# Performance work log

Hardware: AMD Instinct MI355X
Metric: run time of the kernel (lower is better)

## Reference

```python
import jax, jax.numpy as jnp
from jax import lax
import numpy as np

STYLE_STRENGTH = 1.0
PATCH = 3
TOL = 1e-14


def covsqrt_mean(feature, inverse=False):
    # feature: [b, c, h, w]; matches torch covsqrt_mean with eigenvalue truncation.
    b, c, h, w = feature.shape
    f = feature.reshape(b, c, h * w)
    mean = jnp.mean(f, axis=2, keepdims=True)
    zm = f - mean
    cov = jnp.einsum('bcn,bdn->bcd', zm, zm)  # unnormalized covariance, [b,c,c]
    evals, evecs = jnp.linalg.eigh(cov)       # ascending evals, like torch
    p = -0.5 if inverse else 0.5
    # torch keeps evals[k:] where k is the first index with eval > tol; since
    # evals are sorted ascending this equals masking evals > tol.
    mask = evals > TOL
    d = jnp.where(mask, jnp.where(mask, evals, 1.0) ** p, 0.0)
    covsqrt = jnp.einsum('bij,bj,bkj->bik', evecs, d, evecs)
    return covsqrt, mean


def whitening(feature):
    b, c, h, w = feature.shape
    inv_cs, mean = covsqrt_mean(feature, inverse=True)
    out = jnp.einsum('bcd,bdn->bcn', inv_cs, feature.reshape(b, c, -1) - mean)
    return out.reshape(b, c, h, w)


def coloring(feature, target):
    b, c, h, w = feature.shape
    cs, mean = covsqrt_mean(target, inverse=False)
    out = jnp.einsum('bcd,bdn->bcn', cs, feature.reshape(b, c, -1)) + mean
    return out.reshape(b, c, h, w)


def extract_kernels(feat, k):
    # feat [b,c,h,w] -> per-location style patches as conv kernels [b, h*w, c, k, k]
    b, c, h, w = feat.shape
    pad = (k - 1) // 2
    fp = jnp.pad(feat, ((0, 0), (0, 0), (pad, pad), (pad, pad)))
    # stack the k*k shifted views: [b, c, h, w, k*k] in (ky, kx) row-major order,
    # matching torch unfold(2,k).unfold(3,k) flattening.
    patches = jnp.stack([fp[:, :, dy:dy + h, dx:dx + w]
                         for dy in range(k) for dx in range(k)], axis=-1)
    return patches.reshape(b, c, h * w, k * k).transpose(0, 2, 1, 3).reshape(b, h * w, c, k, k)


def reassemble(norm_c, norm_s, k):
    b, c, h, w = norm_c.shape
    ker = extract_kernels(norm_s, k)                                  # [b, hw_s, c, k, k]
    knorm = jnp.sqrt(jnp.sum(ker ** 2, axis=(2, 3, 4), keepdims=True))
    pad = (k - 1) // 2

    def conv_one(feat, kk):
        # feat [c,h,w], kk [hw_s,c,k,k] -> score [hw_s,h,w]
        x = jnp.pad(feat, ((0, 0), (pad, pad), (pad, pad)))[None]
        return lax.conv_general_dilated(x, kk, (1, 1), 'VALID')[0]

    score = jax.vmap(conv_one)(norm_c, ker / knorm)                   # [b, hw_s, h, w]
    idx = jnp.argmax(score, axis=1)                                   # [b, h, w]
    onehot = jax.nn.one_hot(idx, score.shape[1], dtype=score.dtype).transpose(0, 3, 1, 2)

    def deconv_one(oh, kk):
        # conv_transpose2d(padded onehot, kk, padding=k-1) == VALID conv with
        # spatially flipped kernel (in/out channels swapped).
        x = jnp.pad(oh, ((0, 0), (pad, pad), (pad, pad)))[None]        # [1, hw_s, h+2p, w+2p]
        wf = jnp.flip(kk, axis=(2, 3)).transpose(1, 0, 2, 3)           # [c, hw_s, k, k]
        return lax.conv_general_dilated(x, wf, (1, 1), 'VALID')[0]     # [c, h, w]

    out = jax.vmap(deconv_one)(onehot, ker)                           # [b, c, h, w]
    # overlap-count normalization: separable box filter of ones
    cnt_h = jnp.convolve(jnp.ones(h, out.dtype), jnp.ones(k, out.dtype), mode='same')
    cnt_w = jnp.convolve(jnp.ones(w, out.dtype), jnp.ones(k, out.dtype), mode='same')
    deconv_norm = (cnt_h[:, None] * cnt_w[None, :])[None, None]
    return out / deconv_norm


def setup_inputs() -> dict:
    key = jax.random.key(0)
    k1, k2 = jax.random.split(key)
    b, ch, h, w = 2, 256, 48, 48
    c = jax.random.normal(k1, (b, ch, h, w), dtype=jnp.float32)
    s = jax.random.normal(k2, (b, ch, h, w), dtype=jnp.float32)
    return {'c': c, 's': s}


def reference(c, s):
    norm_c = whitening(c)
    norm_s = whitening(s)
    rF = reassemble(norm_c, norm_s, PATCH)
    sF = coloring(rF, s)
    return (1.0 - STYLE_STRENGTH) * c + STYLE_STRENGTH * sF
```

## Files before the change

kernel.cpp:

```cpp
#include <hip/hip_runtime.h>
#include <math.h>

#define HW 2304
#define NC 256
#define NPIX 2500
#define NPIXP 2560
#define MATSZ 65536
#define NS_ITERS 5
#define NSLAB 6
#define KSLAB 384
#define PMSZ (2560 * 256)
#define GSZ ((u64)NPIXP * NPIXP)

typedef unsigned long long u64;
typedef unsigned short ushortt;
typedef __attribute__((ext_vector_type(8))) short bhalf8;
typedef __attribute__((ext_vector_type(4))) float f32x4;

__global__ void mean_kernel(const float* __restrict__ c, const float* __restrict__ s,
                            double* __restrict__ mean, double* __restrict__ snorm) {
  int ch = blockIdx.x, m = blockIdx.y;
  const float* src = (m < 2 ? c + m * (NC * HW) : s + (m - 2) * (NC * HW)) + ch * HW;
  double acc = 0.0, acc2 = 0.0;
  for (int n = threadIdx.x; n < HW; n += 64) {
    double v = (double)src[n];
    acc += v; acc2 += v * v;
  }
  for (int o = 32; o > 0; o >>= 1) {
    acc += __shfl_down(acc, o);
    acc2 += __shfl_down(acc2, o);
  }
  if (threadIdx.x == 0) {
    mean[m * NC + ch] = acc / (double)HW;
    double diag = acc2 - acc * acc / (double)HW;
    atomicAdd(&snorm[m], 1.25 * diag / 256.0);
  }
}

__launch_bounds__(256)
__global__ void cov_part(const float* __restrict__ c, const float* __restrict__ s,
                         float* __restrict__ covp) {
  int z = blockIdx.z;
  int m = z / NSLAB, slab = z % NSLAB;
  const float* src = (m < 2 ? c + m * (NC * HW) : s + (m - 2) * (NC * HW));
  int i0 = blockIdx.y * 64, j0 = blockIdx.x * 64;
  int kb = slab * KSLAB;
  __shared__ float As[16][64], Bs[16][64];
  int tx = threadIdx.x, ty = threadIdx.y;
  int tid = ty * 16 + tx;
  int li = tid >> 2;
  int lk4 = tid & 3;
  float acc[4][4] = {};
  for (int kc = 0; kc < KSLAB; kc += 16) {
    __syncthreads();
    float4 va = *(const float4*)&src[(u64)(i0 + li) * HW + kb + kc + lk4 * 4];
    float4 vb = *(const float4*)&src[(u64)(j0 + li) * HW + kb + kc + lk4 * 4];
    As[lk4 * 4 + 0][li] = va.x; As[lk4 * 4 + 1][li] = va.y;
    As[lk4 * 4 + 2][li] = va.z; As[lk4 * 4 + 3][li] = va.w;
    Bs[lk4 * 4 + 0][li] = vb.x; Bs[lk4 * 4 + 1][li] = vb.y;
    Bs[lk4 * 4 + 2][li] = vb.z; Bs[lk4 * 4 + 3][li] = vb.w;
    __syncthreads();
    #pragma unroll
    for (int kk = 0; kk < 16; ++kk) {
      float4 a = *(const float4*)&As[kk][ty * 4];
      float4 b = *(const float4*)&Bs[kk][tx * 4];
      float av[4] = {a.x, a.y, a.z, a.w};
      float bv[4] = {b.x, b.y, b.z, b.w};
      #pragma unroll
      for (int i = 0; i < 4; ++i)
        #pragma unroll
        for (int j = 0; j < 4; ++j) acc[i][j] += av[i] * bv[j];
    }
  }
  float* Cp = covp + (u64)z * MATSZ;
  #pragma unroll
  for (int i = 0; i < 4; ++i) {
    float4 v = make_float4(acc[i][0], acc[i][1], acc[i][2], acc[i][3]);
    *(float4*)&Cp[(i0 + ty * 4 + i) * NC + j0 + tx * 4] = v;
  }
}

__global__ void cov_reduce(const float* __restrict__ covp, const double* __restrict__ mean,
                           const double* __restrict__ snorm,
                           float* __restrict__ Y0, float* __restrict__ Z1) {
  int m = blockIdx.y;
  int row = blockIdx.x, col = threadIdx.x;
  int e = row * 256 + col;
  float v = 0.0f;
  #pragma unroll
  for (int slab = 0; slab < NSLAB; ++slab)
    v += covp[(u64)(m * NSLAB + slab) * MATSZ + e];
  double mi = mean[m * NC + row], mj = mean[m * NC + col];
  float res = (float)((double)v - (double)HW * mi * mj);
  float inv = (float)(1.0 / snorm[m]);
  float y0 = res * inv;
  Y0[m * MATSZ + e] = y0;
  Z1[m * MATSZ + e] = ((row == col) ? 1.5f : 0.0f) - 0.5f * y0;
}

__launch_bounds__(256)
__global__ void ns_gemm_Y(const float* __restrict__ Y0, const float* __restrict__ T0,
                          float* __restrict__ Y1) {
  int m = blockIdx.z;
  const float* A = Y0 + m * MATSZ;
  const float* B = T0 + m * MATSZ;
  float* Cp = Y1 + m * MATSZ;
  int m0 = blockIdx.y * 32, n0 = blockIdx.x * 32;
  __shared__ float As[32][33], Bs[32][33];
  int tx = threadIdx.x, ty = threadIdx.y;
  int tid = ty * 16 + tx;
  float acc[2][2] = {};
  for (int k0 = 0; k0 < 256; k0 += 32) {
    __syncthreads();
    #pragma unroll
    for (int l = 0; l < 4; ++l) {
      int idx = tid + l * 256;
      int r = idx >> 5, cc = idx & 31;
      As[r][cc] = A[(m0 + r) * NC + k0 + cc];
      Bs[r][cc] = B[(k0 + r) * NC + n0 + cc];
    }
    __syncthreads();
    #pragma unroll
    for (int kk = 0; kk < 32; ++kk) {
      float a0 = As[ty][kk], a1 = As[ty + 16][kk];
      float b0 = Bs[kk][tx], b1 = Bs[kk][tx + 16];
      acc[0][0] += a0 * b0; acc[0][1] += a0 * b1;
      acc[1][0] += a1 * b0; acc[1][1] += a1 * b1;
    }
  }
  #pragma unroll
  for (int i = 0; i < 2; ++i)
    #pragma unroll
    for (int j = 0; j < 2; ++j)
      Cp[(m0 + ty + 16 * i) * NC + n0 + tx + 16 * j] = acc[i][j];
}

__launch_bounds__(256)
__global__ void ns_gemm_T(const float* __restrict__ Zc, const float* __restrict__ Yc,
                          float* __restrict__ T) {
  int m = blockIdx.z;
  const float* A = Zc + m * MATSZ;
  const float* B = Yc + m * MATSZ;
  int m0 = blockIdx.y * 32, n0 = blockIdx.x * 32;
  __shared__ float As[32][33], Bs[32][33];
  int tx = threadIdx.x, ty = threadIdx.y;
  int tid = ty * 16 + tx;
  float acc[2][2] = {};
  for (int k0 = 0; k0 < 256; k0 += 32) {
    __syncthreads();
    #pragma unroll
    for (int l = 0; l < 4; ++l) {
      int idx = tid + l * 256;
      int r = idx >> 5, cc = idx & 31;
      As[r][cc] = A[(m0 + r) * NC + k0 + cc];
      Bs[r][cc] = B[(k0 + r) * NC + n0 + cc];
    }
    __syncthreads();
    #pragma unroll
    for (int kk = 0; kk < 32; ++kk) {
      float a0 = As[ty][kk], a1 = As[ty + 16][kk];
      float b0 = Bs[kk][tx], b1 = Bs[kk][tx + 16];
      acc[0][0] += a0 * b0; acc[0][1] += a0 * b1;
      acc[1][0] += a1 * b0; acc[1][1] += a1 * b1;
    }
  }
  float* Cp = T + m * MATSZ;
  #pragma unroll
  for (int i = 0; i < 2; ++i)
    #pragma unroll
    for (int j = 0; j < 2; ++j) {
      int row = m0 + ty + 16 * i, col = n0 + tx + 16 * j;
      Cp[row * NC + col] = (row == col ? 1.5f : 0.0f) - 0.5f * acc[i][j];
    }
}

__launch_bounds__(256)
__global__ void ns_gemm_YZ(const float* __restrict__ Yc, const float* __restrict__ Zc,
                           const float* __restrict__ T,
                           float* __restrict__ Yn, float* __restrict__ Zn) {
  int z = blockIdx.z;
  int m = z & 3;
  bool isY = (z < 4);
  const float* A = isY ? (Yc + m * MATSZ) : (T + m * MATSZ);
  const float* B = isY ? (T + m * MATSZ) : (Zc + m * MATSZ);
  float* Cp = isY ? (Yn + m * MATSZ) : (Zn + m * MATSZ);
  int m0 = blockIdx.y * 32, n0 = blockIdx.x * 32;
  __shared__ float As[32][33], Bs[32][33];
  int tx = threadIdx.x, ty = threadIdx.y;
  int tid = ty * 16 + tx;
  float acc[2][2] = {};
  for (int k0 = 0; k0 < 256; k0 += 32) {
    __syncthreads();
    #pragma unroll
    for (int l = 0; l < 4; ++l) {
      int idx = tid + l * 256;
      int r = idx >> 5, cc = idx & 31;
      As[r][cc] = A[(m0 + r) * NC + k0 + cc];
      Bs[r][cc] = B[(k0 + r) * NC + n0 + cc];
    }
    __syncthreads();
    #pragma unroll
    for (int kk = 0; kk < 32; ++kk) {
      float a0 = As[ty][kk], a1 = As[ty + 16][kk];
      float b0 = Bs[kk][tx], b1 = Bs[kk][tx + 16];
      acc[0][0] += a0 * b0; acc[0][1] += a0 * b1;
      acc[1][0] += a1 * b0; acc[1][1] += a1 * b1;
    }
  }
  #pragma unroll
  for (int i = 0; i < 2; ++i)
    #pragma unroll
    for (int j = 0; j < 2; ++j)
      Cp[(m0 + ty + 16 * i) * NC + n0 + tx + 16 * j] = acc[i][j];
}

__launch_bounds__(256)
__global__ void whiten_kernel(const float* __restrict__ c, const float* __restrict__ s,
                              const float* __restrict__ Zf,
                              const double* __restrict__ snorm, const double* __restrict__ mean,
                              float* __restrict__ padC_cf, float* __restrict__ padS_cf,
                              float* __restrict__ padS_cl) {
  int mat = blockIdx.z;
  const float* src = (mat < 2 ? c + mat * (NC * HW) : s + (mat - 2) * (NC * HW));
  const float* A = Zf + mat * MATSZ;
  const double* mn = mean + mat * NC;
  float wscale = (float)(1.0 / sqrt(snorm[mat]));
  int m0 = blockIdx.y * 64, n0 = blockIdx.x * 64;
  __shared__ float As[16][68], Bs[16][68];
  int tid = threadIdx.x;
  int tx = tid & 15, ty = tid >> 4;
  int li = tid >> 2, lk4 = tid & 3;
  int kr = tid >> 4, p4 = (tid & 15) * 4;
  float acc[4][4] = {};
  for (int kc = 0; kc < 256; kc += 16) {
    __syncthreads();
    float4 va = *(const float4*)&A[(u64)(m0 + li) * NC + kc + lk4 * 4];
    As[lk4 * 4 + 0][li] = va.x; As[lk4 * 4 + 1][li] = va.y;
    As[lk4 * 4 + 2][li] = va.z; As[lk4 * 4 + 3][li] = va.w;
    float mk = (float)mn[kc + kr];
    float4 vb = *(const float4*)&src[(u64)(kc + kr) * HW + n0 + p4];
    vb.x -= mk; vb.y -= mk; vb.z -= mk; vb.w -= mk;
    *(float4*)&Bs[kr][p4] = vb;
    __syncthreads();
    #pragma unroll
    for (int kk = 0; kk < 16; ++kk) {
      float4 a = *(const float4*)&As[kk][ty * 4];
      float4 b = *(const float4*)&Bs[kk][tx * 4];
      float av[4] = {a.x, a.y, a.z, a.w};
      float bv[4] = {b.x, b.y, b.z, b.w};
      #pragma unroll
      for (int i = 0; i < 4; ++i)
        #pragma unroll
        for (int j = 0; j < 4; ++j) acc[i][j] += av[i] * bv[j];
    }
  }
  #pragma unroll
  for (int i = 0; i < 4; ++i) {
    int row = m0 + ty * 4 + i;
    #pragma unroll
    for (int j = 0; j < 4; ++j) {
      int n = n0 + tx * 4 + j;
      float v = acc[i][j] * wscale;
      int y = n / 48, x = n % 48;
      int ppos = (y + 1) * 50 + (x + 1);
      if (mat < 2) {
        padC_cf[(u64)mat * (NC * NPIXP) + row * NPIXP + ppos] = v;
      } else {
        padS_cf[(u64)(mat - 2) * (NC * NPIXP) + row * NPIXP + ppos] = v;
        padS_cl[(u64)(mat - 2) * (NPIX * NC) + ppos * NC + row] = v;
      }
    }
  }
}

__launch_bounds__(256)
__global__ void tsplit_kernel(const float* __restrict__ padC_cf, const float* __restrict__ padS_cf,
                              ushortt* __restrict__ padCk_hi, ushortt* __restrict__ padCk_lo,
                              ushortt* __restrict__ padSk_hi, ushortt* __restrict__ padSk_lo,
                              float* __restrict__ ssq) {
  int p0 = blockIdx.x * 64;
  int by = blockIdx.y;
  const float* src = (by < 2) ? padC_cf + (u64)by * (NC * NPIXP)
                              : padS_cf + (u64)(by - 2) * (NC * NPIXP);
  ushortt* dhi = (by < 2) ? padCk_hi + (u64)by * PMSZ : padSk_hi + (u64)(by - 2) * PMSZ;
  ushortt* dlo = (by < 2) ? padCk_lo + (u64)by * PMSZ : padSk_lo + (u64)(by - 2) * PMSZ;
  __shared__ float Tk[64][68];
  int tid = threadIdx.x;
  int rr = tid >> 4, c4 = (tid & 15) * 4;
  int p = tid >> 2, kg = (tid & 3) * 16;
  float sq = 0.0f;
  for (int ks = 0; ks < 256; ks += 64) {
    __syncthreads();
    #pragma unroll
    for (int it = 0; it < 4; ++it) {
      int r = rr + it * 16;
      *(float4*)&Tk[r][c4] = *(const float4*)&src[(u64)(ks + r) * NPIXP + p0 + c4];
    }
    __syncthreads();
    __align__(16) ushortt h[16], lo[16];
    #pragma unroll
    for (int e = 0; e < 16; ++e) {
      float v = Tk[kg + e][p];
      sq += v * v;
      unsigned bb = __float_as_uint(v);
      unsigned hu = (bb + 0x7FFFu + ((bb >> 16) & 1u)) >> 16;
      float hf = __uint_as_float(hu << 16);
      float rres = v - hf;
      unsigned lb = __float_as_uint(rres);
      unsigned lu = (lb + 0x7FFFu + ((lb >> 16) & 1u)) >> 16;
      h[e] = (ushortt)hu;
      lo[e] = (ushortt)lu;
    }
    u64 off = (u64)(p0 + p) * 256 + ks + kg;
    *(uint4*)&dhi[off] = *(const uint4*)&h[0];
    *(uint4*)&dhi[off + 8] = *(const uint4*)&h[8];
    *(uint4*)&dlo[off] = *(const uint4*)&lo[0];
    *(uint4*)&dlo[off + 8] = *(const uint4*)&lo[8];
  }
  sq += __shfl_down(sq, 2);
  sq += __shfl_down(sq, 1);
  if (by >= 2 && (tid & 3) == 0 && (p0 + p) < NPIX)
    ssq[(u64)(by - 2) * NPIX + p0 + p] = sq;
}

__launch_bounds__(256)
__global__ void gram_mfma(const ushortt* __restrict__ Ah_b, const ushortt* __restrict__ Al_b,
                          const ushortt* __restrict__ Bh_b, const ushortt* __restrict__ Bl_b,
                          float* __restrict__ Gb) {
  int bz = blockIdx.z;
  const ushortt* Ah_g = Ah_b + (u64)bz * PMSZ;
  const ushortt* Al_g = Al_b + (u64)bz * PMSZ;
  const ushortt* Bh_g = Bh_b + (u64)bz * PMSZ;
  const ushortt* Bl_g = Bl_b + (u64)bz * PMSZ;
  float* G = Gb + (u64)bz * GSZ;
  __shared__ ushortt As_hi[128 * 32], As_lo[128 * 32], Bs_hi[64 * 32], Bs_lo[64 * 32];
  int tid = threadIdx.x;
  int wv = tid >> 6, l = tid & 63, lr = l & 15, lk = l >> 4;
  int p0 = blockIdx.x * 128, q0 = blockIdx.y * 64;
  int arow = tid >> 2;
  int apart = (tid & 3) * 8;
  const ushortt* pAh0 = Ah_g + (u64)(p0 + arow) * 256 + apart;
  const ushortt* pAh1 = Ah_g + (u64)(p0 + arow + 64) * 256 + apart;
  const ushortt* pAl0 = Al_g + (u64)(p0 + arow) * 256 + apart;
  const ushortt* pAl1 = Al_g + (u64)(p0 + arow + 64) * 256 + apart;
  const ushortt* pBh  = Bh_g + (u64)(q0 + arow) * 256 + apart;
  const ushortt* pBl  = Bl_g + (u64)(q0 + arow) * 256 + apart;
  float4 rAh0 = *(const float4*)pAh0;
  float4 rAh1 = *(const float4*)pAh1;
  float4 rAl0 = *(const float4*)pAl0;
  float4 rAl1 = *(const float4*)pAl1;
  float4 rBh  = *(const float4*)pBh;
  float4 rBl  = *(const float4*)pBl;
  f32x4 acc[2][4];
  #pragma unroll
  for (int a = 0; a < 2; ++a)
    #pragma unroll
    for (int b = 0; b < 4; ++b)
      #pragma unroll
      for (int e = 0; e < 4; ++e) acc[a][b][e] = 0.0f;
  for (int k0 = 0; k0 < 256; k0 += 32) {
    __syncthreads();
    *(float4*)&As_hi[arow * 32 + apart] = rAh0;
    *(float4*)&As_hi[(arow + 64) * 32 + apart] = rAh1;
    *(float4*)&As_lo[arow * 32 + apart] = rAl0;
    *(float4*)&As_lo[(arow + 64) * 32 + apart] = rAl1;
    *(float4*)&Bs_hi[arow * 32 + apart] = rBh;
    *(float4*)&Bs_lo[arow * 32 + apart] = rBl;
    __syncthreads();
    if (k0 + 32 < 256) {
      rAh0 = *(const float4*)(pAh0 + k0 + 32);
      rAh1 = *(const float4*)(pAh1 + k0 + 32);
      rAl0 = *(const float4*)(pAl0 + k0 + 32);
      rAl1 = *(const float4*)(pAl1 + k0 + 32);
      rBh  = *(const float4*)(pBh + k0 + 32);
      rBl  = *(const float4*)(pBl + k0 + 32);
    }
    bhalf8 Ah[2], Al[2], Bh[4], Bl[4];
    #pragma unroll
    for (int a = 0; a < 2; ++a) {
      int off = (wv * 32 + a * 16 + lr) * 32 + lk * 8;
      Ah[a] = *(const bhalf8*)&As_hi[off];
      Al[a] = *(const bhalf8*)&As_lo[off];
    }
    #pragma unroll
    for (int b = 0; b < 4; ++b) {
      int off = (b * 16 + lr) * 32 + lk * 8;
      Bh[b] = *(const bhalf8*)&Bs_hi[off];
      Bl[b] = *(const bhalf8*)&Bs_lo[off];
    }
    #pragma unroll
    for (int a = 0; a < 2; ++a)
      #pragma unroll
      for (int b = 0; b < 4; ++b) {
        acc[a][b] = __builtin_amdgcn_mfma_f32_16x16x32_bf16(Ah[a], Bh[b], acc[a][b], 0, 0, 0);
        acc[a][b] = __builtin_amdgcn_mfma_f32_16x16x32_bf16(Ah[a], Bl[b], acc[a][b], 0, 0, 0);
        acc[a][b] = __builtin_amdgcn_mfma_f32_16x16x32_bf16(Al[a], Bh[b], acc[a][b], 0, 0, 0);
      }
  }
  #pragma unroll
  for (int a = 0; a < 2; ++a)
    #pragma unroll
    for (int b = 0; b < 4; ++b)
      #pragma unroll
      for (int r = 0; r < 4; ++r) {
        int p = p0 + wv * 32 + a * 16 + lk * 4 + r;
        int q = q0 + b * 16 + lr;
        G[(u64)p * NPIXP + q] = acc[a][b][r];
      }
}

__launch_bounds__(256)
__global__ void scoremax_kernel(const float* __restrict__ Gb, const float* __restrict__ ssq,
                                u64* __restrict__ rmax) {
  int j = blockIdx.x, cidx = blockIdx.y, b = blockIdx.z;
  int c = cidx - 47;
  int y_lo = c < 0 ? -c : 0;
  int y_hi = c < 0 ? 47 : 47 - c;
  int yt0 = y_lo + j * 4;
  if (yt0 > y_hi) return;
  int ny = min(4, y_hi - yt0 + 1);
  int nb = ny + 2;
  const float* G = Gb + (u64)b * GSZ;
  const float* sq = ssq + (u64)b * NPIX;
  __shared__ float bands[6][2500];
  __shared__ float ssqb[6][52];
  __shared__ float sc[48][52];
  __shared__ float rkl[48];
  int tid = threadIdx.x;
  for (int e = tid; e < nb * 2500; e += 256) {
    int bi = e / 2500, rem = e - bi * 2500;
    int u = rem / 50, v = rem - u * 50;
    int a = yt0 + bi;
    bands[bi][rem] = G[(u64)(a * 50 + u) * NPIXP + (a + c) * 50 + v];
  }
  for (int e = tid; e < nb * 50; e += 256) {
    int bi = e / 50, v = e - bi * 50;
    ssqb[bi][v] = sq[(yt0 + bi + c) * 50 + v];
  }
  __syncthreads();
  for (int jj = 0; jj < ny; ++jj) {
    int y = yt0 + jj, ys = y + c;
    #pragma unroll
    for (int k = 0; k < 9; ++k) {
      int idx = tid + k * 256;
      int x = idx / 48, xs = idx - x * 48;
      float v = 0.0f;
      #pragma unroll
      for (int dy = 0; dy < 3; ++dy)
        #pragma unroll
        for (int dx = 0; dx < 3; ++dx)
          v += bands[jj + dy][(x + dx) * 50 + xs + dx];
      sc[x][xs] = v;
    }
    if (tid < 48) {
      float t = 0.0f;
      #pragma unroll
      for (int dy = 0; dy < 3; ++dy)
        #pragma unroll
        for (int dx = 0; dx < 3; ++dx) t += ssqb[jj + dy][tid + dx];
      rkl[tid] = 1.0f / sqrtf(t);
    }
    __syncthreads();
    if (tid < 192) {
      int r = tid >> 2, part = tid & 3;
      float best = -1e30f; int bxs = 0;
      #pragma unroll
      for (int i = 0; i < 12; ++i) {
        int xs = part * 12 + i;
        float v = sc[r][xs] * rkl[xs];
        if (v > best) { best = v; bxs = xs; }
      }
      #pragma unroll
      for (int o = 1; o < 4; o <<= 1) {
        float ov = __shfl_down(best, o);
        int oi = __shfl_down(bxs, o);
        if (ov > best || (ov == best && oi < bxs)) { best = ov; bxs = oi; }
      }
      if (part == 0) {
        int ps = ys * 48 + bxs;
        unsigned ub = __float_as_uint(best);
        unsigned enc = (ub & 0x80000000u) ? ~ub : (ub | 0x80000000u);
        u64 key = ((u64)enc << 32) | (u64)(2303 - ps);
        atomicMax(&rmax[(u64)b * HW + y * 48 + r], key);
      }
    }
    __syncthreads();
  }
}

__global__ void reassemble_kernel(const float* __restrict__ padS_cl, const u64* __restrict__ rmax,
                                  float* __restrict__ rF_cl) {
  int pix = blockIdx.x, b = blockIdx.y;
  int y = pix / 48, x = pix % 48;
  const u64* rm = rmax + (u64)b * HW;
  const float* S = padS_cl + (u64)b * (NPIX * NC);
  int ch = threadIdx.x;
  float sum = 0.0f;
  #pragma unroll
  for (int i = 0; i < 3; ++i)
    #pragma unroll
    for (int j = 0; j < 3; ++j) {
      int yn = y + 1 - i, xn = x + 1 - j;
      if (yn >= 0 && yn < 48 && xn >= 0 && xn < 48) {
        int ps = 2303 - (int)(unsigned)(rm[yn * 48 + xn] & 0xFFFFFFFFu);
        int ys = ps / 48, xs = ps % 48;
        sum += S[((ys + i) * 50 + xs + j) * NC + ch];
      }
    }
  float cy = (y == 0 || y == 47) ? 2.0f : 3.0f;
  float cx = (x == 0 || x == 47) ? 2.0f : 3.0f;
  rF_cl[(u64)b * (HW * NC) + pix * NC + ch] = sum / (cy * cx);
}

__launch_bounds__(256)
__global__ void coloring_kernel(const float* __restrict__ Yf, const double* __restrict__ snorm,
                                const double* __restrict__ mean, const float* __restrict__ rF_cl,
                                float* __restrict__ out) {
  int b = blockIdx.z;
  const float* A = Yf + (2 + b) * MATSZ;
  const float* Bp = rF_cl + (u64)b * (HW * NC);
  const double* mn = mean + (2 + b) * NC;
  float cscale = (float)sqrt(snorm[2 + b]);
  int m0 = blockIdx.y * 64, n0 = blockIdx.x * 64;
  __shared__ float As[16][68], Bs[16][68];
  int tid = threadIdx.x;
  int tx = tid & 15, ty = tid >> 4;
  int li = tid >> 2, lk4 = tid & 3;
  int pix = tid >> 2, kq = (tid & 3) * 4;
  float acc[4][4] = {};
  for (int kc = 0; kc < 256; kc += 16) {
    __syncthreads();
    float4 va = *(const float4*)&A[(u64)(m0 + li) * NC + kc + lk4 * 4];
    As[lk4 * 4 + 0][li] = va.x; As[lk4 * 4 + 1][li] = va.y;
    As[lk4 * 4 + 2][li] = va.z; As[lk4 * 4 + 3][li] = va.w;
    float4 vb = *(const float4*)&Bp[(u64)(n0 + pix) * NC + kc + kq];
    Bs[kq + 0][pix] = vb.x; Bs[kq + 1][pix] = vb.y;
    Bs[kq + 2][pix] = vb.z; Bs[kq + 3][pix] = vb.w;
    __syncthreads();
    #pragma unroll
    for (int kk = 0; kk < 16; ++kk) {
      float4 a = *(const float4*)&As[kk][ty * 4];
      float4 b2 = *(const float4*)&Bs[kk][tx * 4];
      float av[4] = {a.x, a.y, a.z, a.w};
      float bv[4] = {b2.x, b2.y, b2.z, b2.w};
      #pragma unroll
      for (int i = 0; i < 4; ++i)
        #pragma unroll
        for (int j = 0; j < 4; ++j) acc[i][j] += av[i] * bv[j];
    }
  }
  #pragma unroll
  for (int i = 0; i < 4; ++i) {
    int row = m0 + ty * 4 + i;
    float madd = (float)mn[row];
    float4 v = make_float4(acc[i][0] * cscale + madd, acc[i][1] * cscale + madd,
                           acc[i][2] * cscale + madd, acc[i][3] * cscale + madd);
    *(float4*)&out[(u64)b * (NC * HW) + (u64)row * HW + n0 + tx * 4] = v;
  }
}

extern "C" void kernel_launch(void* const* d_in, const int* in_sizes, int n_in,
                              void* d_out, int out_size, void* d_ws, size_t ws_size,
                              hipStream_t stream) {
  const float* c = (const float*)d_in[0];
  const float* s = (const float*)d_in[1];
  float* out = (float*)d_out;

  char* ws = (char*)d_ws;
  size_t off = 0;
  auto alloc = [&](size_t bytes) {
    void* p = ws + off;
    off = (off + bytes + 255) & ~(size_t)255;
    return p;
  };
  double* mean   = (double*)alloc(4 * NC * sizeof(double));
  float* covp    = (float*)alloc((size_t)4 * NSLAB * MATSZ * sizeof(float));
  float* Ya      = (float*)alloc((size_t)4 * MATSZ * sizeof(float));
  float* Yb      = (float*)alloc((size_t)4 * MATSZ * sizeof(float));
  float* Za      = (float*)alloc((size_t)4 * MATSZ * sizeof(float));
  float* Zb      = (float*)alloc((size_t)4 * MATSZ * sizeof(float));
  float* T       = (float*)alloc((size_t)4 * MATSZ * sizeof(float));
  float* padC_cf = (float*)alloc((size_t)2 * NC * NPIXP * sizeof(float));
  float* padS_cf = (float*)alloc((size_t)2 * NC * NPIXP * sizeof(float));
  float* padS_cl = (float*)alloc((size_t)2 * NPIX * NC * sizeof(float));
  ushortt* padCk_hi = (ushortt*)alloc((size_t)2 * PMSZ * sizeof(ushortt));
  ushortt* padCk_lo = (ushortt*)alloc((size_t)2 * PMSZ * sizeof(ushortt));
  ushortt* padSk_hi = (ushortt*)alloc((size_t)2 * PMSZ * sizeof(ushortt));
  ushortt* padSk_lo = (ushortt*)alloc((size_t)2 * PMSZ * sizeof(ushortt));
  float* ssq     = (float*)alloc((size_t)2 * NPIX * sizeof(float));
  float* rF_cl   = (float*)alloc((size_t)2 * HW * NC * sizeof(float));
  float* G       = (float*)alloc((size_t)2 * GSZ * sizeof(float));
  u64*   rmax    = (u64*)alloc((size_t)2 * HW * sizeof(u64));
  double* snorm  = (double*)alloc(4 * sizeof(double));

  size_t padBytes = (size_t)(2 * NC * NPIXP + 2 * NC * NPIXP + 2 * NPIX * NC) * sizeof(float);
  hipMemsetAsync(padC_cf, 0, padBytes, stream);
  hipMemsetAsync(rmax, 0, (size_t)2 * HW * sizeof(u64) + 4 * sizeof(double), stream);

  mean_kernel<<<dim3(256, 4), 64, 0, stream>>>(c, s, mean, snorm);
  cov_part<<<dim3(4, 4, 4 * NSLAB), dim3(16, 16), 0, stream>>>(c, s, covp);
  cov_reduce<<<dim3(256, 4), 256, 0, stream>>>(covp, mean, snorm, Ya, Za);
  ns_gemm_Y<<<dim3(8, 8, 4), dim3(16, 16), 0, stream>>>(Ya, Za, Yb);

  float *Yc = Yb, *Zc = Za, *Yn = Ya, *Zn = Zb;
  for (int it = 1; it < NS_ITERS; ++it) {
    ns_gemm_T<<<dim3(8, 8, 4), dim3(16, 16), 0, stream>>>(Zc, Yc, T);
    ns_gemm_YZ<<<dim3(8, 8, 8), dim3(16, 16), 0, stream>>>(Yc, Zc, T, Yn, Zn);
    float* t1 = Yc; Yc = Yn; Yn = t1;
    float* t2 = Zc; Zc = Zn; Zn = t2;
  }

  whiten_kernel<<<dim3(36, 4, 4), 256, 0, stream>>>(c, s, Zc, snorm, mean,
                                                    padC_cf, padS_cf, padS_cl);
  tsplit_kernel<<<dim3(40, 4), 256, 0, stream>>>(padC_cf, padS_cf,
                                                 padCk_hi, padCk_lo, padSk_hi, padSk_lo, ssq);

  gram_mfma<<<dim3(20, 40, 2), 256, 0, stream>>>(padCk_hi, padCk_lo, padSk_hi, padSk_lo, G);
  scoremax_kernel<<<dim3(12, 95, 2), 256, 0, stream>>>(G, ssq, rmax);

  reassemble_kernel<<<dim3(2304, 2), 256, 0, stream>>>(padS_cl, rmax, rF_cl);
  coloring_kernel<<<dim3(36, 4, 2), 256, 0, stream>>>(Yc, snorm, mean, rF_cl, out);
}
```

Before: 334.3 us.

## Restructure score-max kernel to one block per row pair with smaller LDS

The score-max kernel now assigns one block to each (content row, style row) pair instead of a diagonal band of up to four rows. It streams the three needed Gram tiles one at a time into a single shared buffer and accumulates the 3x3 patch score in place. This cuts shared memory per block sharply to raise occupancy and doubles the grid size. In exchange, each Gram tile is re-read from global memory more often, since the cross-row band reuse is lost.

```diff
diff --git a/kernel.cpp b/kernel.cpp
--- a/kernel.cpp
+++ b/kernel.cpp
@@ -412,79 +412,64 @@
 __launch_bounds__(256)
 __global__ void scoremax_kernel(const float* __restrict__ Gb, const float* __restrict__ ssq,
                                 u64* __restrict__ rmax) {
-  int j = blockIdx.x, cidx = blockIdx.y, b = blockIdx.z;
-  int c = cidx - 47;
-  int y_lo = c < 0 ? -c : 0;
-  int y_hi = c < 0 ? 47 : 47 - c;
-  int yt0 = y_lo + j * 4;
-  if (yt0 > y_hi) return;
-  int ny = min(4, y_hi - yt0 + 1);
-  int nb = ny + 2;
+  int y = blockIdx.x, ys = blockIdx.y, b = blockIdx.z;
   const float* G = Gb + (u64)b * GSZ;
   const float* sq = ssq + (u64)b * NPIX;
-  __shared__ float bands[6][2500];
-  __shared__ float ssqb[6][52];
+  __shared__ float Gt1[50][52];
   __shared__ float sc[48][52];
+  __shared__ float sr[152];
   __shared__ float rkl[48];
   int tid = threadIdx.x;
-  for (int e = tid; e < nb * 2500; e += 256) {
-    int bi = e / 2500, rem = e - bi * 2500;
-    int u = rem / 50, v = rem - u * 50;
-    int a = yt0 + bi;
-    bands[bi][rem] = G[(u64)(a * 50 + u) * NPIXP + (a + c) * 50 + v];
-  }
-  for (int e = tid; e < nb * 50; e += 256) {
-    int bi = e / 50, v = e - bi * 50;
-    ssqb[bi][v] = sq[(yt0 + bi + c) * 50 + v];
-  }
-  __syncthreads();
-  for (int jj = 0; jj < ny; ++jj) {
-    int y = yt0 + jj, ys = y + c;
+  for (int dy = 0; dy < 3; ++dy) {
+    if (dy > 0) __syncthreads();
+    for (int t = tid; t < 2500; t += 256) {
+      int u = t / 50, v = t - u * 50;
+      Gt1[u][v] = G[(u64)((y + dy) * 50 + u) * NPIXP + (ys + dy) * 50 + v];
+    }
+    if (dy == 0 && tid < 150) {
+      int d = tid / 50, v = tid - d * 50;
+      sr[d * 50 + v] = sq[(ys + d) * 50 + v];
+    }
+    __syncthreads();
+    if (dy == 0 && tid < 48) {
+      float t = 0.0f;
+      #pragma unroll
+      for (int d = 0; d < 3; ++d)
+        #pragma unroll
+        for (int dx = 0; dx < 3; ++dx) t += sr[d * 50 + tid + dx];
+      rkl[tid] = 1.0f / sqrtf(t);
+    }
     #pragma unroll
     for (int k = 0; k < 9; ++k) {
       int idx = tid + k * 256;
       int x = idx / 48, xs = idx - x * 48;
-      float v = 0.0f;
-      #pragma unroll
-      for (int dy = 0; dy < 3; ++dy)
-        #pragma unroll
-        for (int dx = 0; dx < 3; ++dx)
-          v += bands[jj + dy][(x + dx) * 50 + xs + dx];
-      sc[x][xs] = v;
-    }
-    if (tid < 48) {
-      float t = 0.0f;
-      #pragma unroll
-      for (int dy = 0; dy < 3; ++dy)
-        #pragma unroll
-        for (int dx = 0; dx < 3; ++dx) t += ssqb[jj + dy][tid + dx];
-      rkl[tid] = 1.0f / sqrtf(t);
-    }
-    __syncthreads();
-    if (tid < 192) {
-      int r = tid >> 2, part = tid & 3;
-      float best = -1e30f; int bxs = 0;
-      #pragma unroll
-      for (int i = 0; i < 12; ++i) {
-        int xs = part * 12 + i;
-        float v = sc[r][xs] * rkl[xs];
-        if (v > best) { best = v; bxs = xs; }
-      }
-      #pragma unroll
-      for (int o = 1; o < 4; o <<= 1) {
-        float ov = __shfl_down(best, o);
-        int oi = __shfl_down(bxs, o);
-        if (ov > best || (ov == best && oi < bxs)) { best = ov; bxs = oi; }
-      }
-      if (part == 0) {
-        int ps = ys * 48 + bxs;
-        unsigned ub = __float_as_uint(best);
-        unsigned enc = (ub & 0x80000000u) ? ~ub : (ub | 0x80000000u);
-        u64 key = ((u64)enc << 32) | (u64)(2303 - ps);
-        atomicMax(&rmax[(u64)b * HW + y * 48 + r], key);
-      }
-    }
-    __syncthreads();
+      float v = Gt1[x][xs] + Gt1[x + 1][xs + 1] + Gt1[x + 2][xs + 2];
+      sc[x][xs] = (dy == 0) ? v : sc[x][xs] + v;
+    }
+  }
+  __syncthreads();
+  if (tid < 192) {
+    int r = tid >> 2, part = tid & 3;
+    float best = -1e30f; int bxs = 0;
+    #pragma unroll
+    for (int i = 0; i < 12; ++i) {
+      int xs = part * 12 + i;
+      float v = sc[r][xs] * rkl[xs];
+      if (v > best) { best = v; bxs = xs; }
+    }
+    #pragma unroll
+    for (int o = 1; o < 4; o <<= 1) {
+      float ov = __shfl_down(best, o);
+      int oi = __shfl_down(bxs, o);
+      if (ov > best || (ov == best && oi < bxs)) { best = ov; bxs = oi; }
+    }
+    if (part == 0) {
+      int ps = ys * 48 + bxs;
+      unsigned ub = __float_as_uint(best);
+      unsigned enc = (ub & 0x80000000u) ? ~ub : (ub | 0x80000000u);
+      u64 key = ((u64)enc << 32) | (u64)(2303 - ps);
+      atomicMax(&rmax[(u64)b * HW + y * 48 + r], key);
+    }
   }
 }
 
@@ -616,7 +601,7 @@
                                                  padCk_hi, padCk_lo, padSk_hi, padSk_lo, ssq);
 
   gram_mfma<<<dim3(20, 40, 2), 256, 0, stream>>>(padCk_hi, padCk_lo, padSk_hi, padSk_lo, G);
-  scoremax_kernel<<<dim3(12, 95, 2), 256, 0, stream>>>(G, ssq, rmax);
+  scoremax_kernel<<<dim3(48, 48, 2), 256, 0, stream>>>(G, ssq, rmax);
 
   reassemble_kernel<<<dim3(2304, 2), 256, 0, stream>>>(padS_cl, rmax, rF_cl);
   coloring_kernel<<<dim3(36, 4, 2), 256, 0, stream>>>(Yc, snorm, mean, rF_cl, out);
```

New measurement: 316.7 us. 5.3% less time.
